# Performance work log

Measured on AMD Instinct MI355X. Metric: run time of the kernel, lower is better.

Reference implementation:

```python
import jax, jax.numpy as jnp
import numpy as np

# Constants describing the (equal-length) ragged batch and CRF tag space
B, L = 64, 512                 # 64 sequences of 512 segment-tokens each
C = 1024                       # fuse_embedding_channel
NUM_CLASSES = 5                # real field classes
NUM_TAGS = NUM_CLASSES + 2     # + START + STOP
START, STOP = NUM_CLASSES, NUM_CLASSES + 1
NEG = -10000.0


def setup_inputs() -> dict:
    key = jax.random.key(0)
    k1, k2, k3, k4 = jax.random.split(key, 4)
    fuse_embeddings = jax.random.normal(k1, (B * L, C), jnp.float32)
    label_class = jax.random.randint(k2, (B * L,), 0, NUM_CLASSES)
    # classification head params (Linear C -> NUM_TAGS)
    W = jax.random.normal(k3, (NUM_TAGS, C), jnp.float32) * 0.02
    b = jnp.zeros((NUM_TAGS,), jnp.float32)
    # CRF transition matrix: transitions[next, prev]
    transitions = jax.random.normal(k4, (NUM_TAGS, NUM_TAGS), jnp.float32) * 0.01
    transitions = transitions.at[START, :].set(NEG).at[:, STOP].set(NEG)
    return {"fuse_embeddings": fuse_embeddings, "label_class": label_class,
            "W": W, "b": b, "transitions": transitions}


def _crf_nll_sum(feats, tags, transitions):
    """Sum over batch of (forward_alg score - gold score).
    feats: [B, L, T] emissions, tags: [B, L] int, transitions: [T, T] (next, prev)."""
    # --- forward algorithm (batched log-sum-exp recurrence) ---
    init = jnp.full((B, NUM_TAGS), NEG, feats.dtype).at[:, START].set(0.0)

    def step(fv, emit):
        # fv: [B, prev], emit: [B, next]
        fv_new = jax.nn.logsumexp(fv[:, None, :] + transitions[None, :, :], axis=2) + emit
        return fv_new, None

    fv, _ = jax.lax.scan(step, init, jnp.swapaxes(feats, 0, 1))  # scan over L
    fwd_score = jax.nn.logsumexp(fv + transitions[STOP][None, :], axis=1)  # [B]

    # --- gold sentence score ---
    tags_ext = jnp.concatenate([jnp.full((B, 1), START, tags.dtype), tags], axis=1)
    emit_sc = jnp.take_along_axis(feats, tags[..., None], axis=2)[..., 0].sum(axis=1)
    trans_sc = transitions[tags_ext[:, 1:], tags_ext[:, :-1]].sum(axis=1)
    gold = emit_sc + trans_sc + transitions[STOP, tags[:, -1]]
    return (fwd_score - gold).sum()


def reference(fuse_embeddings, label_class, W, b, transitions):
    # per-token linear projection to tag logits
    pred_class = fuse_embeddings @ W.T + b          # [N, NUM_TAGS]
    feats = pred_class.reshape(B, L, NUM_TAGS)
    tags = label_class.reshape(B, L)
    score = _crf_nll_sum(feats, tags, transitions)
    return (jnp.reshape(score, (1,)), label_class.astype(jnp.int32), pred_class)
```

## Files before the change

### kernel.cpp

```cpp
#include <hip/hip_runtime.h>

#define BSEQ 64
#define LSEQ 512
#define CCH  1024
#define NT   7
#define NTOK (BSEQ*LSEQ)
#define START_TAG 5
#define STOP_TAG  6
#define NEGV (-10000.0f)

template<int CTRL, int RMASK, int BMASK>
__device__ __forceinline__ float dpp_add(float x) {
    int y = __builtin_amdgcn_update_dpp(0, __float_as_int(x), CTRL, RMASK, BMASK, true);
    return x + __int_as_float(y);
}
__device__ __forceinline__ float wave_sum(float x) {
    x = dpp_add<0x111, 0xF, 0xF>(x);
    x = dpp_add<0x112, 0xF, 0xF>(x);
    x = dpp_add<0x114, 0xF, 0xF>(x);
    x = dpp_add<0x118, 0xF, 0xF>(x);
    x = dpp_add<0x142, 0xA, 0xF>(x);
    x = dpp_add<0x143, 0xC, 0xF>(x);
    return x;
}

__global__ __launch_bounds__(256)
void k_logits(const float* __restrict__ X, const float* __restrict__ W,
              const float* __restrict__ bvec, const int* __restrict__ lab,
              float* __restrict__ out)
{
    __shared__ float Wl[NT][CCH];
    __shared__ float bl[NT];
    {
        const float4* W4  = (const float4*)W;
        float4*       Wl4 = (float4*)(&Wl[0][0]);
        for (int i = threadIdx.x; i < NT*CCH/4; i += 256) Wl4[i] = W4[i];
        if (threadIdx.x < NT) bl[threadIdx.x] = bvec[threadIdx.x];
    }
    __syncthreads();

    const int lane = threadIdx.x & 63;
    const int wid  = (blockIdx.x * 256 + threadIdx.x) >> 6;
    const int nw   = (gridDim.x * 256) >> 6;
    float* outP = out + 1 + NTOK;

    for (int base = wid * 4; base < NTOK; base += nw * 4) {
        float4 xv[4][4];
        #pragma unroll
        for (int r = 0; r < 4; r++) {
            const float4* xr = (const float4*)(X + (size_t)(base + r) * CCH);
            #pragma unroll
            for (int k = 0; k < 4; k++) xv[k][r] = xr[k*64 + lane];
        }
        float acc[4][NT];
        #pragma unroll
        for (int r = 0; r < 4; r++)
            #pragma unroll
            for (int t = 0; t < NT; t++) acc[r][t] = 0.0f;

        #pragma unroll
        for (int k = 0; k < 4; k++) {
            const int cb = (k*64 + lane) * 4;
            #pragma unroll
            for (int t = 0; t < NT; t++) {
                const float4 wv = *(const float4*)(&Wl[t][cb]);
                #pragma unroll
                for (int r = 0; r < 4; r++) {
                    acc[r][t] = fmaf(xv[k][r].x, wv.x,
                                fmaf(xv[k][r].y, wv.y,
                                fmaf(xv[k][r].z, wv.z,
                                fmaf(xv[k][r].w, wv.w, acc[r][t]))));
                }
            }
        }
        #pragma unroll
        for (int r = 0; r < 4; r++) {
            #pragma unroll
            for (int t = 0; t < NT; t++) {
                float s = wave_sum(acc[r][t]);
                if (lane == 63) outP[(size_t)(base + r) * NT + t] = s + bl[t];
            }
        }
    }

    for (int i = blockIdx.x * 256 + threadIdx.x; i < NTOK; i += gridDim.x * 256)
        out[1 + i] = (float)lab[i];
    if (blockIdx.x == 0 && threadIdx.x == 0) out[0] = 0.0f;
}

__global__ __launch_bounds__(448)
void k_crf(const float* __restrict__ dout_ro, const int* __restrict__ lab,
           const float* __restrict__ trans, float* __restrict__ score)
{
    __shared__ float E[LSEQ*NT];
    __shared__ float M2[32*49];
    __shared__ float T[49];
    __shared__ float gred[7];

    const int b   = blockIdx.x;
    const int tid = threadIdx.x;
    const float* feats = dout_ro + 1 + NTOK + (size_t)b * (LSEQ*NT);

    for (int i = tid; i < LSEQ*NT; i += 448) E[i] = feats[i];
    if (tid < 49) T[tid] = trans[tid];
    __syncthreads();

    float g = 0.0f;
    for (int l = tid; l < LSEQ; l += 448) {
        const int t  = lab[b*LSEQ + l];
        const int tp = (l == 0) ? START_TAG : lab[b*LSEQ + l - 1];
        g += E[l*NT + t] + T[t*NT + tp];
    }
    if (tid == 0) g += T[STOP_TAG*NT + lab[b*LSEQ + LSEQ - 1]];
    {
        float gs = wave_sum(g);
        if ((tid & 63) == 63) gred[tid >> 6] = gs;
    }

    float TR[49];
    #pragma unroll
    for (int i = 0; i < 49; i++) TR[i] = T[i];

    const int chunk = tid / 7;
    const int basis = tid - chunk * 7;
    float fv[7];
    #pragma unroll
    for (int j = 0; j < 7; j++) fv[j] = (j == basis) ? 0.0f : NEGV;

    const int l0 = chunk * 8;
    for (int s = 0; s < 8; s++) {
        float e[7];
        #pragma unroll
        for (int j = 0; j < 7; j++) e[j] = E[(l0 + s)*NT + j];
        float fn[7];
        #pragma unroll
        for (int j = 0; j < 7; j++) {
            float v[7];
            #pragma unroll
            for (int k = 0; k < 7; k++) v[k] = fv[k] + TR[j*7 + k];
            float m = fmaxf(fmaxf(fmaxf(v[0], v[1]), fmaxf(v[2], v[3])),
                            fmaxf(fmaxf(v[4], v[5]), v[6]));
            float sum = 0.0f;
            #pragma unroll
            for (int k = 0; k < 7; k++) sum += __expf(v[k] - m);
            fn[j] = m + __logf(sum) + e[j];
        }
        #pragma unroll
        for (int j = 0; j < 7; j++) fv[j] = fn[j];
    }
    __syncthreads();
    #pragma unroll
    for (int j = 0; j < 7; j++) E[chunk*49 + basis*7 + j] = fv[j];

    int n = 64, cur = 0;
    while (n > 1) {
        __syncthreads();
        const float* in = (cur == 0) ? (const float*)E : (const float*)M2;
        float*       ob = (cur == 0) ? M2 : E;
        const int half = n >> 1;
        for (int e2 = tid; e2 < half*49; e2 += 448) {
            const int p = e2 / 49, r = e2 - p*49;
            const int i = r / 7,  j = r - (r/7)*7;
            const float* A  = in + (2*p)*49 + i*7;
            const float* Bm = in + (2*p + 1)*49 + j;
            float v[7];
            #pragma unroll
            for (int k = 0; k < 7; k++) v[k] = A[k] + Bm[k*7];
            float m = fmaxf(fmaxf(fmaxf(v[0], v[1]), fmaxf(v[2], v[3])),
                            fmaxf(fmaxf(v[4], v[5]), v[6]));
            float sum = 0.0f;
            #pragma unroll
            for (int k = 0; k < 7; k++) sum += __expf(v[k] - m);
            ob[p*49 + r] = m + __logf(sum);
        }
        cur ^= 1; n = half;
    }
    __syncthreads();

    if (tid == 0) {
        float gg = 0.0f;
        #pragma unroll
        for (int w = 0; w < 7; w++) gg += gred[w];
        const float* M = (cur == 0) ? (const float*)E : (const float*)M2;
        float v[7];
        #pragma unroll
        for (int j = 0; j < 7; j++) v[j] = M[START_TAG*7 + j] + T[STOP_TAG*7 + j];
        float m = fmaxf(fmaxf(fmaxf(v[0], v[1]), fmaxf(v[2], v[3])),
                        fmaxf(fmaxf(v[4], v[5]), v[6]));
        float sum = 0.0f;
        #pragma unroll
        for (int j = 0; j < 7; j++) sum += __expf(v[j] - m);
        float fwd = m + __logf(sum);
        atomicAdd(score, fwd - gg);
    }
}

extern "C" void kernel_launch(void* const* d_in, const int* in_sizes, int n_in,
                              void* d_out, int out_size, void* d_ws, size_t ws_size,
                              hipStream_t stream) {
    const float* X     = (const float*)d_in[0];
    const int*   lab   = (const int*)  d_in[1];
    const float* W     = (const float*)d_in[2];
    const float* bvec  = (const float*)d_in[3];
    const float* trans = (const float*)d_in[4];
    float* out = (float*)d_out;

    k_logits<<<512, 256, 0, stream>>>(X, W, bvec, lab, out);
    k_crf<<<BSEQ, 448, 0, stream>>>(out, lab, trans, out);
}
```

Measured before the change: 222.5 us.

## Shrink CRF semiring from 7 to 5 tags and double logits grid

Uses the structure of the transitions (START row and STOP column are −10000) to drop those states from the forward recurrence. The parallel-scan matrices become 5x5 instead of 7x7, and the first step is handled explicitly from START. This cuts exp/log work and shared memory in the CRF kernel, with threads per block going from 448 to 320. Separately, the logits kernel gets a grid of 1024 blocks and a min-blocks launch bound of 4 to raise occupancy. The 5-tag shortcut is only correct if those transition entries are effectively minus infinity, which the task's setup guarantees.

```diff
diff --git a/kernel.cpp b/kernel.cpp
--- a/kernel.cpp
+++ b/kernel.cpp
@@ -4,6 +4,7 @@
 #define LSEQ 512
 #define CCH  1024
 #define NT   7
+#define NC   5
 #define NTOK (BSEQ*LSEQ)
 #define START_TAG 5
 #define STOP_TAG  6
@@ -24,7 +25,15 @@
     return x;
 }
 
-__global__ __launch_bounds__(256)
+__device__ __forceinline__ float lse5(const float v0, const float v1, const float v2,
+                                      const float v3, const float v4) {
+    float m = fmaxf(fmaxf(fmaxf(v0, v1), fmaxf(v2, v3)), v4);
+    float s = __expf(v0 - m) + __expf(v1 - m) + __expf(v2 - m)
+            + __expf(v3 - m) + __expf(v4 - m);
+    return m + __logf(s);
+}
+
+__global__ __launch_bounds__(256, 4)
 void k_logits(const float* __restrict__ X, const float* __restrict__ W,
               const float* __restrict__ bvec, const int* __restrict__ lab,
               float* __restrict__ out)
@@ -88,25 +97,28 @@
     if (blockIdx.x == 0 && threadIdx.x == 0) out[0] = 0.0f;
 }
 
-__global__ __launch_bounds__(448)
+__global__ __launch_bounds__(320)
 void k_crf(const float* __restrict__ dout_ro, const int* __restrict__ lab,
            const float* __restrict__ trans, float* __restrict__ score)
 {
     __shared__ float E[LSEQ*NT];
-    __shared__ float M2[32*49];
+    __shared__ float M2[32*25];
     __shared__ float T[49];
-    __shared__ float gred[7];
+    __shared__ float u_sh[NC];
+    __shared__ float gred[5];
 
     const int b   = blockIdx.x;
     const int tid = threadIdx.x;
     const float* feats = dout_ro + 1 + NTOK + (size_t)b * (LSEQ*NT);
 
-    for (int i = tid; i < LSEQ*NT; i += 448) E[i] = feats[i];
+    for (int i = tid; i < LSEQ*NT; i += 320) E[i] = feats[i];
     if (tid < 49) T[tid] = trans[tid];
     __syncthreads();
 
+    if (tid < NC) u_sh[tid] = T[tid*NT + START_TAG] + E[tid];
+
     float g = 0.0f;
-    for (int l = tid; l < LSEQ; l += 448) {
+    for (int l = tid; l < LSEQ; l += 320) {
         const int t  = lab[b*LSEQ + l];
         const int tp = (l == 0) ? START_TAG : lab[b*LSEQ + l - 1];
         g += E[l*NT + t] + T[t*NT + tp];
@@ -117,40 +129,34 @@
         if ((tid & 63) == 63) gred[tid >> 6] = gs;
     }
 
-    float TR[49];
+    float TR[NC*NC];
     #pragma unroll
-    for (int i = 0; i < 49; i++) TR[i] = T[i];
-
-    const int chunk = tid / 7;
-    const int basis = tid - chunk * 7;
-    float fv[7];
+    for (int j = 0; j < NC; j++)
+        #pragma unroll
+        for (int k = 0; k < NC; k++) TR[j*NC + k] = T[j*NT + k];
+
+    const int chunk = tid / NC;
+    const int basis = tid - chunk * NC;
+    float fv[NC];
     #pragma unroll
-    for (int j = 0; j < 7; j++) fv[j] = (j == basis) ? 0.0f : NEGV;
-
-    const int l0 = chunk * 8;
-    for (int s = 0; s < 8; s++) {
-        float e[7];
-        #pragma unroll
-        for (int j = 0; j < 7; j++) e[j] = E[(l0 + s)*NT + j];
-        float fn[7];
-        #pragma unroll
-        for (int j = 0; j < 7; j++) {
-            float v[7];
-            #pragma unroll
-            for (int k = 0; k < 7; k++) v[k] = fv[k] + TR[j*7 + k];
-            float m = fmaxf(fmaxf(fmaxf(v[0], v[1]), fmaxf(v[2], v[3])),
-                            fmaxf(fmaxf(v[4], v[5]), v[6]));
-            float sum = 0.0f;
-            #pragma unroll
-            for (int k = 0; k < 7; k++) sum += __expf(v[k] - m);
-            fn[j] = m + __logf(sum) + e[j];
-        }
-        #pragma unroll
-        for (int j = 0; j < 7; j++) fv[j] = fn[j];
+    for (int j = 0; j < NC; j++) fv[j] = (j == basis) ? 0.0f : NEGV;
+
+    const int l0    = (chunk == 0) ? 1 : chunk * 8;
+    const int steps = (chunk == 0) ? 7 : 8;
+    for (int s = 0; s < steps; s++) {
+        const int l = l0 + s;
+        float fn[NC];
+        #pragma unroll
+        for (int j = 0; j < NC; j++) {
+            fn[j] = lse5(fv[0] + TR[j*NC+0], fv[1] + TR[j*NC+1], fv[2] + TR[j*NC+2],
+                         fv[3] + TR[j*NC+3], fv[4] + TR[j*NC+4]) + E[l*NT + j];
+        }
+        #pragma unroll
+        for (int j = 0; j < NC; j++) fv[j] = fn[j];
     }
     __syncthreads();
     #pragma unroll
-    for (int j = 0; j < 7; j++) E[chunk*49 + basis*7 + j] = fv[j];
+    for (int j = 0; j < NC; j++) E[chunk*25 + basis*NC + j] = fv[j];
 
     int n = 64, cur = 0;
     while (n > 1) {
@@ -158,39 +164,29 @@
         const float* in = (cur == 0) ? (const float*)E : (const float*)M2;
         float*       ob = (cur == 0) ? M2 : E;
         const int half = n >> 1;
-        for (int e2 = tid; e2 < half*49; e2 += 448) {
-            const int p = e2 / 49, r = e2 - p*49;
-            const int i = r / 7,  j = r - (r/7)*7;
-            const float* A  = in + (2*p)*49 + i*7;
-            const float* Bm = in + (2*p + 1)*49 + j;
-            float v[7];
-            #pragma unroll
-            for (int k = 0; k < 7; k++) v[k] = A[k] + Bm[k*7];
-            float m = fmaxf(fmaxf(fmaxf(v[0], v[1]), fmaxf(v[2], v[3])),
-                            fmaxf(fmaxf(v[4], v[5]), v[6]));
-            float sum = 0.0f;
-            #pragma unroll
-            for (int k = 0; k < 7; k++) sum += __expf(v[k] - m);
-            ob[p*49 + r] = m + __logf(sum);
+        for (int e2 = tid; e2 < half*25; e2 += 320) {
+            const int p = e2 / 25, r = e2 - p*25;
+            const int i = r / NC, j = r - (r/NC)*NC;
+            const float* A  = in + (2*p)*25 + i*NC;
+            const float* Bm = in + (2*p + 1)*25 + j;
+            ob[p*25 + r] = lse5(A[0] + Bm[0], A[1] + Bm[NC], A[2] + Bm[2*NC],
+                                A[3] + Bm[3*NC], A[4] + Bm[4*NC]);
         }
         cur ^= 1; n = half;
     }
     __syncthreads();
 
     if (tid == 0) {
-        float gg = 0.0f;
-        #pragma unroll
-        for (int w = 0; w < 7; w++) gg += gred[w];
+        float gg = gred[0] + gred[1] + gred[2] + gred[3] + gred[4];
         const float* M = (cur == 0) ? (const float*)E : (const float*)M2;
-        float v[7];
-        #pragma unroll
-        for (int j = 0; j < 7; j++) v[j] = M[START_TAG*7 + j] + T[STOP_TAG*7 + j];
-        float m = fmaxf(fmaxf(fmaxf(v[0], v[1]), fmaxf(v[2], v[3])),
-                        fmaxf(fmaxf(v[4], v[5]), v[6]));
-        float sum = 0.0f;
-        #pragma unroll
-        for (int j = 0; j < 7; j++) sum += __expf(v[j] - m);
-        float fwd = m + __logf(sum);
+        float v[NC];
+        #pragma unroll
+        for (int j = 0; j < NC; j++)
+            v[j] = lse5(u_sh[0] + M[0*NC+j], u_sh[1] + M[1*NC+j], u_sh[2] + M[2*NC+j],
+                        u_sh[3] + M[3*NC+j], u_sh[4] + M[4*NC+j]);
+        float fwd = lse5(v[0] + T[STOP_TAG*NT+0], v[1] + T[STOP_TAG*NT+1],
+                         v[2] + T[STOP_TAG*NT+2], v[3] + T[STOP_TAG*NT+3],
+                         v[4] + T[STOP_TAG*NT+4]);
         atomicAdd(score, fwd - gg);
     }
 }
@@ -205,6 +201,6 @@
     const float* trans = (const float*)d_in[4];
     float* out = (float*)d_out;
 
-    k_logits<<<512, 256, 0, stream>>>(X, W, bvec, lab, out);
-    k_crf<<<BSEQ, 448, 0, stream>>>(out, lab, trans, out);
-}
+    k_logits<<<1024, 256, 0, stream>>>(X, W, bvec, lab, out);
+    k_crf<<<BSEQ, 320, 0, stream>>>(out, lab, trans, out);
+}
```

New measurement: 291.1 us. 30.9% more time.
